# Performance work log

Measured on AMD Instinct MI355X. Metric: run time of the kernel, lower is better.

Reference implementation:

```python
import jax, jax.numpy as jnp
from jax import lax
import numpy as np

P, N, C, S = 16, 128, 256, 64
HID = C // 4  # squeeze_ratio = 4
NEG_SLOPE = 0.01  # nn.LeakyReLU default


def setup_inputs() -> dict:
    key = jax.random.key(0)
    k = jax.random.split(key, 5)
    sc = 0.05
    return {
        "x": jax.random.normal(k[0], (P, N, C, S), jnp.float32),
        "w1a": jax.random.normal(k[1], (P, HID, C, 3), jnp.float32) * sc,
        "w1b": jax.random.normal(k[2], (P, C, HID, 1), jnp.float32) * sc,
        "w3a": jax.random.normal(k[3], (P, HID, C, 3), jnp.float32) * sc,
        "w3b": jax.random.normal(k[4], (P, C, HID, 3), jnp.float32) * sc,
    }


def _conv1d(x, w, pad):
    # x: [n, c_in, s], w: [c_out, c_in, k] -> [n, c_out, s]
    return lax.conv_general_dilated(
        x, w, window_strides=(1,), padding=[(pad, pad)],
        dimension_numbers=("NCH", "OIH", "NCH"))


def _leaky(z):
    return jnp.where(z >= 0, z, NEG_SLOPE * z)


def _avg_pool(x, k, pad):
    # PyTorch AvgPool1d default count_include_pad=True: divide by k everywhere.
    s = lax.reduce_window(x, 0.0, lax.add, (1, 1, k), (1, 1, 1),
                          [(0, 0), (0, 0), (pad, pad)])
    return s / k


def _max_pool(x, k, pad):
    return lax.reduce_window(x, -jnp.inf, lax.max, (1, 1, k), (1, 1, 1),
                             [(0, 0), (0, 0), (pad, pad)])


def reference(x, w1a, w1b, w3a, w3b):
    p, n, c, s = x.shape
    xf = x.reshape(p * n, c, s)

    # 3x1 branch: per-part Conv1d(c->hid,k3,p1) -> LeakyReLU -> Conv1d(hid->c,k1,p0)
    logits3x1 = jax.vmap(
        lambda xi, a, b: _conv1d(_leaky(_conv1d(xi, a, 1)), b, 0))(x, w1a, w1b)
    feat3x1 = (_avg_pool(xf, 3, 1) + _max_pool(xf, 3, 1)).reshape(p, n, c, s)
    feat3x1 = feat3x1 * jax.nn.sigmoid(logits3x1)

    # 3x3 branch: per-part Conv1d(c->hid,k3,p1) -> LeakyReLU -> Conv1d(hid->c,k3,p1)
    logits3x3 = jax.vmap(
        lambda xi, a, b: _conv1d(_leaky(_conv1d(xi, a, 1)), b, 1))(x, w3a, w3b)
    feat3x3 = (_avg_pool(xf, 5, 2) + _max_pool(xf, 5, 2)).reshape(p, n, c, s)
    feat3x3 = feat3x3 * jax.nn.sigmoid(logits3x3)

    # fused temporal max over s -> [p, n, c]
    return jnp.max(feat3x1 + feat3x3, axis=-1)
```

## Files before the change

### kernel.cpp

```cpp
#include <hip/hip_runtime.h>
#include <hip/hip_bf16.h>

#define PARTS 16
#define NB 128
#define CH 256
#define SL 64
#define HIDN 64

typedef unsigned short u16;
typedef unsigned int u32;
typedef unsigned short ushort8 __attribute__((ext_vector_type(8)));
typedef unsigned short ushort4v __attribute__((ext_vector_type(4)));
typedef __attribute__((ext_vector_type(8))) short short8v;
typedef __attribute__((ext_vector_type(4))) float f32x4;

__device__ __forceinline__ float bf2f(u16 u) {
  union { unsigned u; float f; } t; t.u = ((unsigned)u) << 16; return t.f;
}
__device__ __forceinline__ u16 f2bf(float f) {
  union { float f; unsigned u; } t; t.f = f;
  unsigned u = t.u;
  u += 0x7FFFu + ((u >> 16) & 1u);
  return (u16)(u >> 16);
}
__device__ __forceinline__ unsigned pk2bf(float a, float b) {
  float2 f; f.x = a; f.y = b;
  union { __hip_bfloat162 h; unsigned u; } cv;
  cv.h = __float22bfloat162_rn(f);
  return cv.u;
}

__global__ void cvt_tap(const float* __restrict__ in, u16* __restrict__ out, int NT) {
  const int i = blockIdx.x * 256 + threadIdx.x;
  const int p = i >> 14, xid = i & 16383;
  const float* src = in + (size_t)i * NT;
  for (int t = 0; t < NT; ++t)
    out[(size_t)(p * NT + t) * 16384 + xid] = f2bf(src[t]);
}

__device__ __forceinline__ int xsw(int r, int c) { return (r * 256 + c) ^ ((r & 7) << 3); }
__device__ __forceinline__ int hsw(int r, int c) { return (r * 64 + c) ^ ((r & 7) << 3); }

__global__ __launch_bounds__(256, 2) void tfa_mfma(
    const float* __restrict__ x,
    const u16* __restrict__ wsb,
    float* __restrict__ out)
{
  const u16* W1A = wsb;
  const u16* W3A = wsb + 786432;
  const u16* W1B = wsb + 1572864;
  const u16* W3B = wsb + 1835008;

  __shared__ __attribute__((aligned(16))) u16 xt[64 * 256];
  __shared__ __attribute__((aligned(16))) u16 ht[64 * 64];

  const int tid = threadIdx.x;
  const int bid = blockIdx.x;
  const int p = bid >> 7;
  const int lane = tid & 63;
  const int w = tid >> 6;

  {
    const float* xb = x + (size_t)bid * (CH * SL);
    const int s = lane;
    #pragma unroll
    for (int j = 0; j < 8; ++j) {
      const int c0 = w * 64 + j * 8;
      union { ushort8 v; unsigned u[4]; } ov;
      #pragma unroll
      for (int k = 0; k < 4; ++k) {
        const float fa = xb[(c0 + 2 * k) * 64 + s];
        const float fb = xb[(c0 + 2 * k + 1) * 64 + s];
        ov.u[k] = pk2bf(fa, fb);
      }
      *(ushort8*)&xt[xsw(s, c0)] = ov.v;
    }
  }
  __syncthreads();

  const int cm = lane & 15;
  const int kg = lane >> 4;

  u32 H3pk[4][2];
  {
    const int h = w * 16 + cm;
    f32x4 acc1[4], acc3[4];
    #pragma unroll
    for (int nt = 0; nt < 4; ++nt) { acc1[nt] = (f32x4)0.f; acc3[nt] = (f32x4)0.f; }

    #pragma unroll 2
    for (int ks = 0; ks < 8; ++ks) {
      const int kc = ks * 32 + kg * 8;
      short8v a1[3], a3[3];
      #pragma unroll
      for (int t = 0; t < 3; ++t) {
        a1[t] = *(const short8v*)&W1A[(size_t)((p * 3 + t) * 64 + h) * 256 + kc];
        a3[t] = *(const short8v*)&W3A[(size_t)((p * 3 + t) * 64 + h) * 256 + kc];
      }
      #pragma unroll
      for (int nt = 0; nt < 4; ++nt) {
        const int s = nt * 16 + cm;
        #pragma unroll
        for (int t = 0; t < 3; ++t) {
          const int r = s + t - 1;
          const bool oob = (unsigned)r > 63u;
          const short8v bb = *(const short8v*)&xt[xsw(oob ? s : r, kc)];
          const short8v b = oob ? (short8v)(short)0 : bb;
          acc1[nt] = __builtin_amdgcn_mfma_f32_16x16x32_bf16(a1[t], b, acc1[nt], 0, 0, 0);
          acc3[nt] = __builtin_amdgcn_mfma_f32_16x16x32_bf16(a3[t], b, acc3[nt], 0, 0, 0);
        }
      }
    }

    const int hc = w * 16 + kg * 4;
    #pragma unroll
    for (int nt = 0; nt < 4; ++nt) {
      const int s = nt * 16 + cm;
      float v1[4], v3[4];
      #pragma unroll
      for (int q = 0; q < 4; ++q) {
        const float a = acc1[nt][q]; v1[q] = a >= 0.f ? a : 0.01f * a;
        const float bq = acc3[nt][q]; v3[q] = bq >= 0.f ? bq : 0.01f * bq;
      }
      union { ushort4v v; u32 u[2]; } o1;
      o1.u[0] = pk2bf(v1[0], v1[1]); o1.u[1] = pk2bf(v1[2], v1[3]);
      *(ushort4v*)&ht[hsw(s, hc)] = o1.v;
      H3pk[nt][0] = pk2bf(v3[0], v3[1]); H3pk[nt][1] = pk2bf(v3[2], v3[3]);
    }
  }
  __syncthreads();

  u32 g1p[4][4][2];
  #pragma unroll
  for (int half = 0; half < 2; ++half) {
    f32x4 acc[2][4];
    #pragma unroll
    for (int mt = 0; mt < 2; ++mt)
      #pragma unroll
      for (int nt = 0; nt < 4; ++nt) acc[mt][nt] = (f32x4)0.f;

    #pragma unroll
    for (int ks = 0; ks < 2; ++ks) {
      const int kh = ks * 32 + kg * 8;
      short8v a[2];
      #pragma unroll
      for (int mt = 0; mt < 2; ++mt) {
        const int c = w * 64 + (half * 2 + mt) * 16 + cm;
        a[mt] = *(const short8v*)&W1B[((size_t)p * 256 + c) * 64 + kh];
      }
      #pragma unroll
      for (int nt = 0; nt < 4; ++nt) {
        const int s = nt * 16 + cm;
        const short8v b = *(const short8v*)&ht[hsw(s, kh)];
        #pragma unroll
        for (int mt = 0; mt < 2; ++mt)
          acc[mt][nt] = __builtin_amdgcn_mfma_f32_16x16x32_bf16(a[mt], b, acc[mt][nt], 0, 0, 0);
      }
    }
    #pragma unroll
    for (int mt = 0; mt < 2; ++mt)
      #pragma unroll
      for (int nt = 0; nt < 4; ++nt) {
        #pragma unroll
        for (int j = 0; j < 2; ++j) {
          const float ga = 1.f / (1.f + __expf(-acc[mt][nt][2 * j]));
          const float gb = 1.f / (1.f + __expf(-acc[mt][nt][2 * j + 1]));
          g1p[half * 2 + mt][nt][j] = pk2bf(ga, gb);
        }
      }
  }
  __syncthreads();

  {
    const int hc = w * 16 + kg * 4;
    #pragma unroll
    for (int nt = 0; nt < 4; ++nt) {
      const int s = nt * 16 + cm;
      union { ushort4v v; u32 u[2]; } o3;
      o3.u[0] = H3pk[nt][0]; o3.u[1] = H3pk[nt][1];
      *(ushort4v*)&ht[hsw(s, hc)] = o3.v;
    }
  }
  __syncthreads();

  #pragma unroll 1
  for (int half = 0; half < 2; ++half) {
    f32x4 acc[2][4];
    #pragma unroll
    for (int mt = 0; mt < 2; ++mt)
      #pragma unroll
      for (int nt = 0; nt < 4; ++nt) acc[mt][nt] = (f32x4)0.f;

    #pragma unroll
    for (int ks = 0; ks < 2; ++ks) {
      const int kh = ks * 32 + kg * 8;
      #pragma unroll
      for (int t = 0; t < 3; ++t) {
        short8v a[2];
        #pragma unroll
        for (int mt = 0; mt < 2; ++mt) {
          const int c = w * 64 + (half * 2 + mt) * 16 + cm;
          a[mt] = *(const short8v*)&W3B[(size_t)((p * 3 + t) * 256 + c) * 64 + kh];
        }
        #pragma unroll
        for (int nt = 0; nt < 4; ++nt) {
          const int s = nt * 16 + cm;
          const int r = s + t - 1;
          const bool oob = (unsigned)r > 63u;
          const short8v bb = *(const short8v*)&ht[hsw(oob ? s : r, kh)];
          const short8v b = oob ? (short8v)(short)0 : bb;
          #pragma unroll
          for (int mt = 0; mt < 2; ++mt)
            acc[mt][nt] = __builtin_amdgcn_mfma_f32_16x16x32_bf16(a[mt], b, acc[mt][nt], 0, 0, 0);
        }
      }
    }

    #pragma unroll
    for (int mt = 0; mt < 2; ++mt) {
      const int c4 = w * 64 + (half * 2 + mt) * 16 + kg * 4;
      float fmx0 = -INFINITY, fmx1 = -INFINITY, fmx2 = -INFINITY, fmx3 = -INFINITY;
      #pragma unroll
      for (int nt = 0; nt < 4; ++nt) {
        const int sg = nt * 16 + cm;
        const int rm2 = sg >= 2 ? sg - 2 : 0;
        const int rm1 = sg >= 1 ? sg - 1 : 0;
        const int rp1 = sg <= 62 ? sg + 1 : 63;
        const int rp2 = sg <= 61 ? sg + 2 : 63;
        const ushort4v vm2 = *(const ushort4v*)&xt[xsw(rm2, c4)];
        const ushort4v vm1 = *(const ushort4v*)&xt[xsw(rm1, c4)];
        const ushort4v v0  = *(const ushort4v*)&xt[xsw(sg,  c4)];
        const ushort4v vp1 = *(const ushort4v*)&xt[xsw(rp1, c4)];
        const ushort4v vp2 = *(const ushort4v*)&xt[xsw(rp2, c4)];
        const float NI = -INFINITY;
        float ft[4];
        #pragma unroll
        for (int q = 0; q < 4; ++q) {
          const float xm2r = bf2f(vm2[q]), xm1r = bf2f(vm1[q]), x0 = bf2f(v0[q]);
          const float xp1r = bf2f(vp1[q]), xp2r = bf2f(vp2[q]);
          const float am2 = sg >= 2 ? xm2r : 0.f;
          const float am1 = sg >= 1 ? xm1r : 0.f;
          const float ap1 = sg <= 62 ? xp1r : 0.f;
          const float ap2 = sg <= 61 ? xp2r : 0.f;
          const float mx3 = fmaxf(x0, fmaxf(sg >= 1 ? xm1r : NI, sg <= 62 ? xp1r : NI));
          const float mx5 = fmaxf(mx3, fmaxf(sg >= 2 ? xm2r : NI, sg <= 61 ? xp2r : NI));
          const float av3 = (am1 + x0 + ap1) * (1.f / 3.f);
          const float av5 = (am2 + am1 + x0 + ap1 + ap2) * 0.2f;
          const float g1 = bf2f((u16)(g1p[half * 2 + mt][nt][q >> 1] >> ((q & 1) * 16)));
          const float g3 = 1.f / (1.f + __expf(-acc[mt][nt][q]));
          ft[q] = (av3 + mx3) * g1 + (av5 + mx5) * g3;
        }
        fmx0 = fmaxf(fmx0, ft[0]); fmx1 = fmaxf(fmx1, ft[1]);
        fmx2 = fmaxf(fmx2, ft[2]); fmx3 = fmaxf(fmx3, ft[3]);
      }
      #pragma unroll
      for (int off = 1; off < 16; off <<= 1) {
        fmx0 = fmaxf(fmx0, __shfl_xor(fmx0, off));
        fmx1 = fmaxf(fmx1, __shfl_xor(fmx1, off));
        fmx2 = fmaxf(fmx2, __shfl_xor(fmx2, off));
        fmx3 = fmaxf(fmx3, __shfl_xor(fmx3, off));
      }
      if (cm == 0) {
        float4 o; o.x = fmx0; o.y = fmx1; o.z = fmx2; o.w = fmx3;
        *(float4*)&out[(size_t)bid * 256 + c4] = o;
      }
    }
  }
}

#define XROW 72
#define HROW 72

__global__ __launch_bounds__(256, 2) void tfa_kernel(
    const float* __restrict__ x,
    const float* __restrict__ w1a,
    const float* __restrict__ w1b,
    const float* __restrict__ w3a,
    const float* __restrict__ w3b,
    float* __restrict__ out)
{
  __shared__ __attribute__((aligned(16))) u16 x_s[8 + CH * XROW];
  __shared__ __attribute__((aligned(16))) u16 h1_s[8 + HIDN * HROW];
  __shared__ __attribute__((aligned(16))) u16 h3_s[8 + HIDN * HROW];

  const int tid = threadIdx.x;
  const int bid = blockIdx.x;
  const int p = bid >> 7;

  {
    const ushort8 z = {0, 0, 0, 0, 0, 0, 0, 0};
    for (int i = tid; i < 257; i += 256) {
      u16* dst = (i == 0) ? &x_s[0] : &x_s[8 + (i - 1) * XROW + 64];
      *(ushort8*)dst = z;
    }
    if (tid < 65) {
      u16* d1 = (tid == 0) ? &h1_s[0] : &h1_s[8 + (tid - 1) * HROW + 64];
      *(ushort8*)d1 = z;
      u16* d3 = (tid == 0) ? &h3_s[0] : &h3_s[8 + (tid - 1) * HROW + 64];
      *(ushort8*)d3 = z;
    }
  }

  const float* xblk = x + (size_t)bid * (CH * SL);
  #pragma unroll
  for (int j = 0; j < 16; ++j) {
    const int g = tid + 256 * j;
    const float4 v = ((const float4*)xblk)[g];
    const int c = g >> 4, s4 = g & 15;
    ushort4v o;
    o[0] = f2bf(v.x); o[1] = f2bf(v.y); o[2] = f2bf(v.z); o[3] = f2bf(v.w);
    *(ushort4v*)&x_s[8 + c * XROW + s4 * 4] = o;
  }
  __syncthreads();

  {
    const int h = tid >> 2;
    const int sg = tid & 3;
    const int sb = sg << 4;
    float acc1[16], acc3[16];
    #pragma unroll
    for (int i = 0; i < 16; ++i) { acc1[i] = 0.f; acc3[i] = 0.f; }

    const float* w1a_p = w1a + ((size_t)p * HIDN + h) * (CH * 3);
    const float* w3a_p = w3a + ((size_t)p * HIDN + h) * (CH * 3);

    for (int c4 = 0; c4 < CH; c4 += 4) {
      const float4 a0v = *(const float4*)&w1a_p[c4 * 3];
      const float4 a1v = *(const float4*)&w1a_p[c4 * 3 + 4];
      const float4 a2v = *(const float4*)&w1a_p[c4 * 3 + 8];
      const float4 b0v = *(const float4*)&w3a_p[c4 * 3];
      const float4 b1v = *(const float4*)&w3a_p[c4 * 3 + 4];
      const float4 b2v = *(const float4*)&w3a_p[c4 * 3 + 8];
      float wa[12], wb[12];
      wa[0]=a0v.x; wa[1]=a0v.y; wa[2]=a0v.z; wa[3]=a0v.w;
      wa[4]=a1v.x; wa[5]=a1v.y; wa[6]=a1v.z; wa[7]=a1v.w;
      wa[8]=a2v.x; wa[9]=a2v.y; wa[10]=a2v.z; wa[11]=a2v.w;
      wb[0]=b0v.x; wb[1]=b0v.y; wb[2]=b0v.z; wb[3]=b0v.w;
      wb[4]=b1v.x; wb[5]=b1v.y; wb[6]=b1v.z; wb[7]=b1v.w;
      wb[8]=b2v.x; wb[9]=b2v.y; wb[10]=b2v.z; wb[11]=b2v.w;

      #pragma unroll
      for (int cc = 0; cc < 4; ++cc) {
        const int c = c4 + cc;
        const ushort8 w0v = *(const ushort8*)&x_s[c * XROW + sb];
        const ushort8 w1v = *(const ushort8*)&x_s[c * XROW + sb + 8];
        const ushort8 w2v = *(const ushort8*)&x_s[c * XROW + sb + 16];
        const ushort8 w3v = *(const ushort8*)&x_s[c * XROW + sb + 24];
        float xf[19];
        xf[0] = bf2f(w0v[7]);
        #pragma unroll
        for (int d = 0; d < 8; ++d) xf[1 + d] = bf2f(w1v[d]);
        #pragma unroll
        for (int d = 0; d < 8; ++d) xf[9 + d] = bf2f(w2v[d]);
        xf[17] = bf2f(w3v[0]);
        xf[18] = bf2f(w3v[1]);

        const float a0 = wa[cc * 3], a1 = wa[cc * 3 + 1], a2 = wa[cc * 3 + 2];
        const float b0 = wb[cc * 3], b1 = wb[cc * 3 + 1], b2 = wb[cc * 3 + 2];
        #pragma unroll
        for (int i = 0; i < 16; ++i) {
          const float xm = xf[i], x0 = xf[i + 1], xp = xf[i + 2];
          acc1[i] = fmaf(a0, xm, fmaf(a1, x0, fmaf(a2, xp, acc1[i])));
          acc3[i] = fmaf(b0, xm, fmaf(b1, x0, fmaf(b2, xp, acc3[i])));
        }
      }
    }

    ushort8 o1a, o1b, o3a, o3b;
    #pragma unroll
    for (int i = 0; i < 8; ++i) {
      float v1 = acc1[i];     v1 = v1 >= 0.f ? v1 : 0.01f * v1;
      float v3 = acc3[i];     v3 = v3 >= 0.f ? v3 : 0.01f * v3;
      o1a[i] = f2bf(v1); o3a[i] = f2bf(v3);
      float u1 = acc1[i + 8]; u1 = u1 >= 0.f ? u1 : 0.01f * u1;
      float u3 = acc3[i + 8]; u3 = u3 >= 0.f ? u3 : 0.01f * u3;
      o1b[i] = f2bf(u1); o3b[i] = f2bf(u3);
    }
    *(ushort8*)&h1_s[8 + h * HROW + sb]     = o1a;
    *(ushort8*)&h1_s[8 + h * HROW + sb + 8] = o1b;
    *(ushort8*)&h3_s[8 + h * HROW + sb]     = o3a;
    *(ushort8*)&h3_s[8 + h * HROW + sb + 8] = o3b;
  }
  __syncthreads();

  {
    const int lane = tid & 63;
    const int wid = __builtin_amdgcn_readfirstlane(tid >> 6);
    const int s = lane;
    const float* w1b_p = w1b + (size_t)p * (CH * HIDN);
    const float* w3b_p = w3b + (size_t)p * (CH * HIDN * 3);
    float* outp = out + (size_t)bid * CH;

    for (int q = 0; q < 16; ++q) {
      const int c0 = wid * 64 + q * 4;
      float l1[4] = {0.f, 0.f, 0.f, 0.f};
      float l3[4] = {0.f, 0.f, 0.f, 0.f};

      for (int h4 = 0; h4 < HIDN; h4 += 4) {
        float h1v[4], h3a[4], h3b[4], h3c[4];
        #pragma unroll
        for (int u = 0; u < 4; ++u) {
          const int hh = h4 + u;
          h1v[u] = bf2f(h1_s[8 + hh * HROW + s]);
          h3a[u] = bf2f(h3_s[7 + hh * HROW + s]);
          h3b[u] = bf2f(h3_s[8 + hh * HROW + s]);
          h3c[u] = bf2f(h3_s[9 + hh * HROW + s]);
        }
        #pragma unroll
        for (int j = 0; j < 4; ++j) {
          const int c = c0 + j;
          const float4 wv  = *(const float4*)&w1b_p[c * HIDN + h4];
          const float* w3  = &w3b_p[(size_t)(c * HIDN + h4) * 3];
          const float4 w30 = *(const float4*)w3;
          const float4 w31 = *(const float4*)(w3 + 4);
          const float4 w32 = *(const float4*)(w3 + 8);
          float ww[12];
          ww[0]=w30.x; ww[1]=w30.y; ww[2]=w30.z; ww[3]=w30.w;
          ww[4]=w31.x; ww[5]=w31.y; ww[6]=w31.z; ww[7]=w31.w;
          ww[8]=w32.x; ww[9]=w32.y; ww[10]=w32.z; ww[11]=w32.w;
          l1[j] = fmaf(wv.x, h1v[0], fmaf(wv.y, h1v[1],
                  fmaf(wv.z, h1v[2], fmaf(wv.w, h1v[3], l1[j]))));
          #pragma unroll
          for (int u = 0; u < 4; ++u) {
            l3[j] = fmaf(ww[u * 3], h3a[u],
                    fmaf(ww[u * 3 + 1], h3b[u],
                    fmaf(ww[u * 3 + 2], h3c[u], l3[j])));
          }
        }
      }

      #pragma unroll
      for (int j = 0; j < 4; ++j) {
        const int c = c0 + j;
        const u16* xr = &x_s[8 + c * XROW];
        const float xm2 = bf2f(xr[s - 2]);
        const float xm1 = bf2f(xr[s - 1]);
        const float x0  = bf2f(xr[s]);
        const float xp1 = bf2f(xr[s + 1]);
        const float xp2 = bf2f(xr[s + 2]);
        const float NI = -INFINITY;
        const float mx3 = fmaxf(x0, fmaxf(s >= 1 ? xm1 : NI, s <= 62 ? xp1 : NI));
        const float mx5 = fmaxf(mx3, fmaxf(s >= 2 ? xm2 : NI, s <= 61 ? xp2 : NI));
        const float av3 = (xm1 + x0 + xp1) * (1.f / 3.f);
        const float av5 = (xm2 + xm1 + x0 + xp1 + xp2) * 0.2f;
        const float sg1 = 1.f / (1.f + __expf(-l1[j]));
        const float sg3 = 1.f / (1.f + __expf(-l3[j]));
        float feat = (av3 + mx3) * sg1 + (av5 + mx5) * sg3;
        #pragma unroll
        for (int off = 32; off >= 1; off >>= 1)
          feat = fmaxf(feat, __shfl_xor(feat, off));
        if (lane == 0) outp[c] = feat;
      }
    }
  }
}

extern "C" void kernel_launch(void* const* d_in, const int* in_sizes, int n_in,
                              void* d_out, int out_size, void* d_ws, size_t ws_size,
                              hipStream_t stream) {
  (void)in_sizes; (void)n_in; (void)out_size;
  const float* x   = (const float*)d_in[0];
  const float* w1a = (const float*)d_in[1];
  const float* w1b = (const float*)d_in[2];
  const float* w3a = (const float*)d_in[3];
  const float* w3b = (const float*)d_in[4];
  float* out = (float*)d_out;

  const size_t WS_NEED = 2621440ull * 2ull;
  if (ws_size >= WS_NEED) {
    u16* wsb = (u16*)d_ws;
    cvt_tap<<<1024, 256, 0, stream>>>(w1a, wsb,           3);
    cvt_tap<<<1024, 256, 0, stream>>>(w3a, wsb + 786432,  3);
    cvt_tap<<<1024, 256, 0, stream>>>(w1b, wsb + 1572864, 1);
    cvt_tap<<<1024, 256, 0, stream>>>(w3b, wsb + 1835008, 3);
    tfa_mfma<<<PARTS * NB, 256, 0, stream>>>(x, wsb, out);
  } else {
    tfa_kernel<<<PARTS * NB, 256, 0, stream>>>(x, w1a, w1b, w3a, w3b, out);
  }
}
```

Before: 136.9 us.

## Use padded zero-halo LDS layout and fuse the two second-stage gate passes

```diff
diff --git a/kernel.cpp b/kernel.cpp
--- a/kernel.cpp
+++ b/kernel.cpp
@@ -38,8 +38,8 @@
     out[(size_t)(p * NT + t) * 16384 + xid] = f2bf(src[t]);
 }
 
-__device__ __forceinline__ int xsw(int r, int c) { return (r * 256 + c) ^ ((r & 7) << 3); }
-__device__ __forceinline__ int hsw(int r, int c) { return (r * 64 + c) ^ ((r & 7) << 3); }
+#define XSTR 264
+#define HSTR 72
 
 __global__ __launch_bounds__(256, 2) void tfa_mfma(
     const float* __restrict__ x,
@@ -51,8 +51,9 @@
   const u16* W1B = wsb + 1572864;
   const u16* W3B = wsb + 1835008;
 
-  __shared__ __attribute__((aligned(16))) u16 xt[64 * 256];
-  __shared__ __attribute__((aligned(16))) u16 ht[64 * 64];
+  __shared__ __attribute__((aligned(16))) u16 xt[68 * XSTR];
+  __shared__ __attribute__((aligned(16))) u16 ht1[64 * HSTR];
+  __shared__ __attribute__((aligned(16))) u16 ht3[64 * HSTR];
 
   const int tid = threadIdx.x;
   const int bid = blockIdx.x;
@@ -60,6 +61,13 @@
   const int lane = tid & 63;
   const int w = tid >> 6;
 
+  if (tid < 132) {
+    const int r4 = tid / 33;
+    const int chunk = tid - r4 * 33;
+    const int r = (r4 < 2) ? r4 : r4 + 64;
+    *(ushort8*)&xt[r * XSTR + chunk * 8] = (ushort8)0;
+  }
+
   {
     const float* xb = x + (size_t)bid * (CH * SL);
     const int s = lane;
@@ -73,7 +81,7 @@
         const float fb = xb[(c0 + 2 * k + 1) * 64 + s];
         ov.u[k] = pk2bf(fa, fb);
       }
-      *(ushort8*)&xt[xsw(s, c0)] = ov.v;
+      *(ushort8*)&xt[(s + 2) * XSTR + c0] = ov.v;
     }
   }
   __syncthreads();
@@ -81,7 +89,6 @@
   const int cm = lane & 15;
   const int kg = lane >> 4;
 
-  u32 H3pk[4][2];
   {
     const int h = w * 16 + cm;
     f32x4 acc1[4], acc3[4];
@@ -102,10 +109,7 @@
         const int s = nt * 16 + cm;
         #pragma unroll
         for (int t = 0; t < 3; ++t) {
-          const int r = s + t - 1;
-          const bool oob = (unsigned)r > 63u;
-          const short8v bb = *(const short8v*)&xt[xsw(oob ? s : r, kc)];
-          const short8v b = oob ? (short8v)(short)0 : bb;
+          const short8v b = *(const short8v*)&xt[(s + t + 1) * XSTR + kc];
           acc1[nt] = __builtin_amdgcn_mfma_f32_16x16x32_bf16(a1[t], b, acc1[nt], 0, 0, 0);
           acc3[nt] = __builtin_amdgcn_mfma_f32_16x16x32_bf16(a3[t], b, acc3[nt], 0, 0, 0);
         }
@@ -122,16 +126,16 @@
         const float a = acc1[nt][q]; v1[q] = a >= 0.f ? a : 0.01f * a;
         const float bq = acc3[nt][q]; v3[q] = bq >= 0.f ? bq : 0.01f * bq;
       }
-      union { ushort4v v; u32 u[2]; } o1;
+      union { ushort4v v; u32 u[2]; } o1, o3;
       o1.u[0] = pk2bf(v1[0], v1[1]); o1.u[1] = pk2bf(v1[2], v1[3]);
-      *(ushort4v*)&ht[hsw(s, hc)] = o1.v;
-      H3pk[nt][0] = pk2bf(v3[0], v3[1]); H3pk[nt][1] = pk2bf(v3[2], v3[3]);
+      o3.u[0] = pk2bf(v3[0], v3[1]); o3.u[1] = pk2bf(v3[2], v3[3]);
+      *(ushort4v*)&ht1[s * HSTR + hc] = o1.v;
+      *(ushort4v*)&ht3[s * HSTR + hc] = o3.v;
     }
   }
   __syncthreads();
 
-  u32 g1p[4][4][2];
-  #pragma unroll
+  #pragma unroll 1
   for (int half = 0; half < 2; ++half) {
     f32x4 acc[2][4];
     #pragma unroll
@@ -151,12 +155,14 @@
       #pragma unroll
       for (int nt = 0; nt < 4; ++nt) {
         const int s = nt * 16 + cm;
-        const short8v b = *(const short8v*)&ht[hsw(s, kh)];
+        const short8v b = *(const short8v*)&ht1[s * HSTR + kh];
         #pragma unroll
         for (int mt = 0; mt < 2; ++mt)
           acc[mt][nt] = __builtin_amdgcn_mfma_f32_16x16x32_bf16(a[mt], b, acc[mt][nt], 0, 0, 0);
       }
     }
+
+    u32 g1p[2][4][2];
     #pragma unroll
     for (int mt = 0; mt < 2; ++mt)
       #pragma unroll
@@ -165,31 +171,10 @@
         for (int j = 0; j < 2; ++j) {
           const float ga = 1.f / (1.f + __expf(-acc[mt][nt][2 * j]));
           const float gb = 1.f / (1.f + __expf(-acc[mt][nt][2 * j + 1]));
-          g1p[half * 2 + mt][nt][j] = pk2bf(ga, gb);
-        }
-      }
-  }
-  __syncthreads();
-
-  {
-    const int hc = w * 16 + kg * 4;
-    #pragma unroll
-    for (int nt = 0; nt < 4; ++nt) {
-      const int s = nt * 16 + cm;
-      union { ushort4v v; u32 u[2]; } o3;
-      o3.u[0] = H3pk[nt][0]; o3.u[1] = H3pk[nt][1];
-      *(ushort4v*)&ht[hsw(s, hc)] = o3.v;
-    }
-  }
-  __syncthreads();
-
-  #pragma unroll 1
-  for (int half = 0; half < 2; ++half) {
-    f32x4 acc[2][4];
-    #pragma unroll
-    for (int mt = 0; mt < 2; ++mt)
-      #pragma unroll
-      for (int nt = 0; nt < 4; ++nt) acc[mt][nt] = (f32x4)0.f;
+          g1p[mt][nt][j] = pk2bf(ga, gb);
+        }
+        acc[mt][nt] = (f32x4)0.f;
+      }
 
     #pragma unroll
     for (int ks = 0; ks < 2; ++ks) {
@@ -207,7 +192,7 @@
           const int s = nt * 16 + cm;
           const int r = s + t - 1;
           const bool oob = (unsigned)r > 63u;
-          const short8v bb = *(const short8v*)&ht[hsw(oob ? s : r, kh)];
+          const short8v bb = *(const short8v*)&ht3[(oob ? s : r) * HSTR + kh];
           const short8v b = oob ? (short8v)(short)0 : bb;
           #pragma unroll
           for (int mt = 0; mt < 2; ++mt)
@@ -223,30 +208,22 @@
       #pragma unroll
       for (int nt = 0; nt < 4; ++nt) {
         const int sg = nt * 16 + cm;
-        const int rm2 = sg >= 2 ? sg - 2 : 0;
-        const int rm1 = sg >= 1 ? sg - 1 : 0;
-        const int rp1 = sg <= 62 ? sg + 1 : 63;
-        const int rp2 = sg <= 61 ? sg + 2 : 63;
-        const ushort4v vm2 = *(const ushort4v*)&xt[xsw(rm2, c4)];
-        const ushort4v vm1 = *(const ushort4v*)&xt[xsw(rm1, c4)];
-        const ushort4v v0  = *(const ushort4v*)&xt[xsw(sg,  c4)];
-        const ushort4v vp1 = *(const ushort4v*)&xt[xsw(rp1, c4)];
-        const ushort4v vp2 = *(const ushort4v*)&xt[xsw(rp2, c4)];
+        const ushort4v vm2 = *(const ushort4v*)&xt[(sg)     * XSTR + c4];
+        const ushort4v vm1 = *(const ushort4v*)&xt[(sg + 1) * XSTR + c4];
+        const ushort4v v0  = *(const ushort4v*)&xt[(sg + 2) * XSTR + c4];
+        const ushort4v vp1 = *(const ushort4v*)&xt[(sg + 3) * XSTR + c4];
+        const ushort4v vp2 = *(const ushort4v*)&xt[(sg + 4) * XSTR + c4];
         const float NI = -INFINITY;
         float ft[4];
         #pragma unroll
         for (int q = 0; q < 4; ++q) {
-          const float xm2r = bf2f(vm2[q]), xm1r = bf2f(vm1[q]), x0 = bf2f(v0[q]);
-          const float xp1r = bf2f(vp1[q]), xp2r = bf2f(vp2[q]);
-          const float am2 = sg >= 2 ? xm2r : 0.f;
-          const float am1 = sg >= 1 ? xm1r : 0.f;
-          const float ap1 = sg <= 62 ? xp1r : 0.f;
-          const float ap2 = sg <= 61 ? xp2r : 0.f;
-          const float mx3 = fmaxf(x0, fmaxf(sg >= 1 ? xm1r : NI, sg <= 62 ? xp1r : NI));
-          const float mx5 = fmaxf(mx3, fmaxf(sg >= 2 ? xm2r : NI, sg <= 61 ? xp2r : NI));
-          const float av3 = (am1 + x0 + ap1) * (1.f / 3.f);
-          const float av5 = (am2 + am1 + x0 + ap1 + ap2) * 0.2f;
-          const float g1 = bf2f((u16)(g1p[half * 2 + mt][nt][q >> 1] >> ((q & 1) * 16)));
+          const float xm2 = bf2f(vm2[q]), xm1 = bf2f(vm1[q]), x0 = bf2f(v0[q]);
+          const float xp1 = bf2f(vp1[q]), xp2 = bf2f(vp2[q]);
+          const float mx3 = fmaxf(x0, fmaxf(sg >= 1 ? xm1 : NI, sg <= 62 ? xp1 : NI));
+          const float mx5 = fmaxf(mx3, fmaxf(sg >= 2 ? xm2 : NI, sg <= 61 ? xp2 : NI));
+          const float av3 = (xm1 + x0 + xp1) * (1.f / 3.f);
+          const float av5 = (xm2 + xm1 + x0 + xp1 + xp2) * 0.2f;
+          const float g1 = bf2f((u16)(g1p[mt][nt][q >> 1] >> ((q & 1) * 16)));
           const float g3 = 1.f / (1.f + __expf(-acc[mt][nt][q]));
           ft[q] = (av3 + mx3) * g1 + (av5 + mx5) * g3;
         }
```

Result: no change. 136.1 us (-0.6%).
